# Optimization experiments

Hardware: AMD Instinct MI355X
Metric: run time of the kernel (lower is better)

## Reference

```python
import jax, jax.numpy as jnp
import numpy as np

N_NODES, NUM_FEAT, EMB, HID, N_CLASSES, N_EDGES = 800, 111, 32, 200, 15, 8000
ALPHA = 0.5   # DirGNNConv default mixing
EPS = 1e-5    # LayerNorm eps


def _pade_coeffs(deg=5):
    # [5/5] Pade approximant of sqrt(1 - x) (as in FastDifferentiableMatSqrt)
    K = 2 * deg + 1
    b = np.zeros(K); b[0] = 1.0
    for k in range(1, K):
        b[k] = b[k - 1] * (0.5 - (k - 1)) / k
    c = b * ((-1.0) ** np.arange(K))  # Taylor coeffs of sqrt(1-x)
    A = np.empty((deg, deg))
    for i in range(deg):
        for j in range(1, deg + 1):
            A[i, j - 1] = c[deg + 1 + i - j]
    q = np.concatenate([[1.0], np.linalg.solve(A, -c[deg + 1:])])
    p = np.array([sum(q[j] * c[k - j] for j in range(min(k, deg) + 1)) for k in range(deg + 1)])
    return p.astype(np.float32), q.astype(np.float32)

PADE_P, PADE_Q = _pade_coeffs()


def _mpa_impl(A):
    # matrix square root via Pade approximant (MPA forward)
    normA = jnp.sqrt(jnp.sum(A * A))
    I = jnp.eye(A.shape[0], dtype=A.dtype)
    p_app = I - A / normA
    p_hat = p_app
    p_sqrt = PADE_P[0] * I
    q_sqrt = PADE_Q[0] * I
    for i in range(5):
        p_sqrt = p_sqrt + PADE_P[i + 1] * p_hat
        q_sqrt = q_sqrt + PADE_Q[i + 1] * p_hat
        p_hat = p_hat @ p_app
    return jnp.linalg.solve(q_sqrt, p_sqrt) * jnp.sqrt(normA)


@jax.custom_vjp
def mpa_lya(A):
    return _mpa_impl(A)


def _mpa_fwd(A):
    S = _mpa_impl(A)
    return S, (S, jnp.sqrt(jnp.sum(A * A)))


def _mpa_bwd(res, g):
    # iterative Lyapunov solver backward (8 coupled Newton-Schulz iterations)
    S, normA = res
    I = jnp.eye(S.shape[0], dtype=S.dtype)
    b = S / jnp.sqrt(normA)
    c = g / jnp.sqrt(normA)
    for _ in range(8):
        b2 = b @ b
        c = 0.5 * (c @ (3.0 * I - b2) - b2 @ c + b @ (c @ b))
        b = 0.5 * (b @ (3.0 * I - b2))
    return (0.5 * c,)

mpa_lya.defvjp(_mpa_fwd, _mpa_bwd)


def gcn_sparse(m, ei, n):
    # GCNConv(normalize=False): out[dst] = sum_{(src,dst) in E} (x @ W)[src]
    return jax.ops.segment_sum(m[ei[0]], ei[1], num_segments=n)


def hetero_layer_sparse(h, eis, W, b):
    # W: [3(in,out,root), 4 edge types, Fin, Fout]; HeteroConv aggr='sum'
    n = h.shape[0]
    out = jnp.zeros((n, W.shape[-1]), h.dtype)
    for e, ei in enumerate(eis):
        x_in = gcn_sparse(h @ W[0, e], ei, n) + b[0, e]
        x_out = gcn_sparse(h @ W[1, e], ei[::-1], n) + b[1, e]  # flipped edges
        out = out + ALPHA * x_out + (1.0 - ALPHA) * x_in + h @ W[2, e] + b[2, e]
    return out


def hetero_layer_dense(h, masks, W, b):
    # masks: [4, N, N] binary adjacency (src, dst); dense equivalent of scatter
    out = jnp.zeros((h.shape[0], W.shape[-1]), h.dtype)
    for e in range(masks.shape[0]):
        x_in = masks[e].T @ (h @ W[0, e]) + b[0, e]
        x_out = masks[e] @ (h @ W[1, e]) + b[1, e]
        out = out + ALPHA * x_out + (1.0 - ALPHA) * x_in + h @ W[2, e] + b[2, e]
    return out


def graph_layernorm(h, wb):
    # PyG LayerNorm mode='graph', single graph: normalize over all nodes+feats
    mu = jnp.mean(h)
    var = jnp.mean((h - mu) ** 2)
    return (h - mu) / jnp.sqrt(var + EPS) * wb[0] + wb[1]


def hetero_gnn(h, layer_fn, graph, W1, b1, W2, b2, ln):
    h = graph_layernorm(layer_fn(h, graph, W1, b1), ln[0])
    return graph_layernorm(layer_fn(h, graph, W2, b2), ln[1])


def pairwise_S(z, lin_W, lin_b, iu, ju):
    n = z.shape[0]
    M = (z[iu] - z[ju]) ** 2                        # [N(N+1)/2, HID]
    mg = jax.nn.sigmoid(M @ lin_W + lin_b)[:, 0]    # upper-tri entries, row-major
    tri = jnp.zeros((n, n), z.dtype).at[iu, ju].set(mg)
    return mpa_lya(tri)


def model_forward(x_note, embed_W, embed_b, g1_l1_W, g1_l1_b, g1_l2_W, g1_l2_b, g1_ln,
                  g2_l1_W, g2_l1_b, g2_l2_W, g2_l2_b, g2_ln, lin_W, lin_b, clf_W, clf_b,
                  eis, batch):
    n = x_note.shape[0]
    iu, ju = np.triu_indices(n)
    h = x_note @ embed_W + embed_b                   # [N, 32]
    z0 = hetero_gnn(h, hetero_layer_sparse, eis, g1_l1_W, g1_l1_b, g1_l2_W, g1_l2_b, g1_ln)
    S1 = pairwise_S(z0, lin_W, lin_b, iu, ju)
    A0 = jnp.stack([jnp.zeros((n, n), h.dtype).at[ei[0], ei[1]].set(1.0) for ei in eis])
    h = S1 @ h
    # adj_to_coord(nonzero) only keeps the binary pattern of S1 @ A @ S1
    mask1 = jnp.stack([((S1 @ A0[e]) @ S1 != 0).astype(h.dtype) for e in range(4)])
    z1 = hetero_gnn(h, hetero_layer_dense, mask1, g2_l1_W, g2_l1_b, g2_l2_W, g2_l2_b, g2_ln)
    S2 = pairwise_S(z1, lin_W, lin_b, iu, ju)
    h = S2 @ h
    mask2 = jnp.stack([((S2 @ mask1[e]) @ S2 != 0).astype(h.dtype) for e in range(4)])
    z2 = hetero_gnn(h, hetero_layer_dense, mask2, g2_l1_W, g2_l1_b, g2_l2_W, g2_l2_b, g2_ln)
    counts = jax.ops.segment_sum(jnp.ones((n,), z2.dtype), batch, num_segments=1)
    x2 = jax.ops.segment_sum(z2, batch, num_segments=1) / counts[:, None]  # global_mean_pool
    logits = x2 @ clf_W + clf_b
    return x2, jax.nn.log_softmax(logits, axis=-1), S1, S2


def setup_inputs() -> dict:
    key = jax.random.key(0)
    ks = jax.random.split(key, 14)
    N, F, E, H, NC, NE = N_NODES, NUM_FEAT, EMB, HID, N_CLASSES, N_EDGES
    def w(k, shape, fan_in):
        return (jax.random.normal(k, shape, jnp.float32) / np.sqrt(fan_in)).astype(jnp.float32)
    ln = jnp.broadcast_to(jnp.stack([jnp.ones(H, jnp.float32), jnp.zeros(H, jnp.float32)]), (2, 2, H)) + 0.0
    return dict(
        x_note=jax.random.normal(ks[0], (N, F), jnp.float32),
        embed_W=w(ks[1], (F, E), F), embed_b=jnp.zeros((E,), jnp.float32),
        g1_l1_W=w(ks[2], (3, 4, E, H), E), g1_l1_b=jnp.zeros((3, 4, H), jnp.float32),
        g1_l2_W=w(ks[3], (3, 4, H, H), H), g1_l2_b=jnp.zeros((3, 4, H), jnp.float32),
        g1_ln=ln,
        g2_l1_W=w(ks[4], (3, 4, E, H), E), g2_l1_b=jnp.zeros((3, 4, H), jnp.float32),
        g2_l2_W=w(ks[5], (3, 4, H, H), H), g2_l2_b=jnp.zeros((3, 4, H), jnp.float32),
        g2_ln=ln,
        lin_W=w(ks[6], (H, 1), H), lin_b=jnp.zeros((1,), jnp.float32),
        clf_W=w(ks[7], (H, NC), H), clf_b=jnp.zeros((NC,), jnp.float32),
        ei_forward=jax.random.randint(ks[8], (2, NE), 0, N, jnp.int32),
        ei_onset=jax.random.randint(ks[9], (2, NE), 0, N, jnp.int32),
        ei_sustain=jax.random.randint(ks[10], (2, NE), 0, N, jnp.int32),
        ei_rest=jax.random.randint(ks[11], (2, NE), 0, N, jnp.int32),
        batch=jnp.zeros((N,), jnp.int32),
    )


def reference(x_note, embed_W, embed_b, g1_l1_W, g1_l1_b, g1_l2_W, g1_l2_b, g1_ln,
              g2_l1_W, g2_l1_b, g2_l2_W, g2_l2_b, g2_ln, lin_W, lin_b, clf_W, clf_b,
              ei_forward, ei_onset, ei_sustain, ei_rest, batch):
    eis = (ei_forward, ei_onset, ei_sustain, ei_rest)
    return model_forward(x_note, embed_W, embed_b, g1_l1_W, g1_l1_b, g1_l2_W, g1_l2_b, g1_ln,
                         g2_l1_W, g2_l1_b, g2_l2_W, g2_l2_b, g2_ln, lin_W, lin_b, clf_W, clf_b,
                         eis, batch)
```

## Files before the change

kernel.cpp:

```cpp
#include <hip/hip_runtime.h>
#include <hip/hip_bf16.h>
#include <math.h>
#include <stdio.h>

static constexpr int   kN  = 800;
static constexpr int   kF  = 111;
static constexpr int   kE  = 32;
static constexpr int   kH  = 200;
static constexpr int   kNC = 15;
static constexpr int   kNE = 8000;
static constexpr long  kNN = (long)kN*kN;
static constexpr long  kNH = (long)kN*kH;
static constexpr float kAl  = 0.5f;
static constexpr float kEps = 1e-5f;
static constexpr int   kGB  = (int)((kNH+255)/256);
static constexpr int   kDB  = 50;

typedef unsigned short u16;
typedef __attribute__((ext_vector_type(8))) short short8;
typedef __attribute__((ext_vector_type(4))) float f32x4;

__device__ __forceinline__ u16 f2bf(float v){
  __hip_bfloat16 b = __float2bfloat16(v);
  return *reinterpret_cast<u16*>(&b);
}
__device__ __forceinline__ float bf2f(u16 h){
  unsigned int u = ((unsigned int)h) << 16;
  float f; __builtin_memcpy(&f, &u, 4);
  return f;
}

enum { EPI_NONE=0, EPI_BIAS=1, EPI_SCALE=4, EPI_ACC=6 };

template<bool TRANSA, bool TRIUA, bool TRIUB, int EPI>
__global__ __launch_bounds__(256)
void gemm_kernel(const float* __restrict__ A, int lda,
                 const float* __restrict__ B, int ldb,
                 float* __restrict__ C, int ldc,
                 int M, int Ncl, int K,
                 long sA, long sB, long sC, float scale,
                 const float* __restrict__ bias, int kstep,
                 const double* __restrict__ scalp)
{
  constexpr int TM=64, TN=64, TK=16;
  A += (long)blockIdx.z * sA;
  B += (long)blockIdx.z * sB;
  C += (long)blockIdx.z * sC;
  __shared__ float As[TK][TM+4];
  __shared__ float Bs[TK][TN+4];
  const int tid = threadIdx.x;
  const int tn4 = (tid & 15)*4, tm4 = (tid >> 4)*4;
  const int m0 = blockIdx.x * TM, n0 = blockIdx.y * TN;
  float acc[4][4] = {};
  const int kbase = kstep ? (int)blockIdx.z * kstep : 0;
  int k0 = TRIUA ? max(m0 - kbase, 0) : 0;
  int kEnd = TRIUB ? min(K, n0 + TN - kbase) : K;
  const bool skip = (k0 >= kEnd);
  if (skip && EPI == EPI_ACC) return;
  if (!skip) {
    float ar[4], br[4];
    auto loadT = [&](int kk0, float* arr, float* brr){
      #pragma unroll
      for (int u=0; u<4; ++u){
        int idx = tid + 256*u;
        float av;
        if (!TRANSA) {
          int m = idx >> 4, ka = idx & 15;
          int gm = m0+m, gk = kk0+ka;
          av = (gm < M && gk < K) ? A[(long)gm*lda + gk] : 0.f;
        } else {
          int ka = idx >> 6, m = idx & 63;
          int gm = m0+m, gk = kk0+ka;
          av = (gm < M && gk < K) ? A[(long)gk*lda + gm] : 0.f;
        }
        int kb = idx >> 6, nb = idx & 63;
        int gk = kk0+kb, gn = n0+nb;
        arr[u] = av;
        brr[u] = (gk < K && gn < Ncl) ? B[(long)gk*ldb + gn] : 0.f;
      }
    };
    auto storeT = [&](const float* arr, const float* brr){
      #pragma unroll
      for (int u=0; u<4; ++u){
        int idx = tid + 256*u;
        if (!TRANSA){ int m = idx>>4, ka = idx&15; As[ka][m] = arr[u]; }
        else        { int ka = idx>>6, m = idx&63; As[ka][m] = arr[u]; }
        int kb = idx>>6, nb = idx&63;
        Bs[kb][nb] = brr[u];
      }
    };
    loadT(k0, ar, br);
    for (;;){
      __syncthreads();
      storeT(ar, br);
      __syncthreads();
      int kn = k0 + TK;
      bool more = kn < kEnd;
      if (more) loadT(kn, ar, br);
      #pragma unroll
      for (int kk=0; kk<TK; ++kk) {
        float a[4], b[4];
        #pragma unroll
        for (int u=0;u<4;++u){ a[u]=As[kk][tm4+u]; b[u]=Bs[kk][tn4+u]; }
        #pragma unroll
        for (int i=0;i<4;++i)
          #pragma unroll
          for (int j=0;j<4;++j)
            acc[i][j] = fmaf(a[i], b[j], acc[i][j]);
      }
      if (!more) break;
      k0 = kn;
    }
  }
  float sc = scale;
  if (EPI == EPI_ACC && scalp) sc *= (float)sqrt(sqrt(scalp[0]));
  #pragma unroll
  for (int i=0;i<4;++i) {
    int gm = m0 + tm4 + i;
    if (gm >= M) continue;
    #pragma unroll
    for (int j=0;j<4;++j) {
      int gn = n0 + tn4 + j;
      if (gn >= Ncl) continue;
      float v = acc[i][j];
      long off = (long)gm*ldc + gn;
      if (EPI == EPI_BIAS)       C[off] = v + bias[gn];
      else if (EPI == EPI_SCALE) C[off] = scale*v;
      else if (EPI == EPI_ACC)   unsafeAtomicAdd(&C[off], sc*v);
      else                       C[off] = v;
    }
  }
}

template<bool TRANSA, bool TRIUA, bool TRIUB, int EPI>
static inline void launch_gemm(hipStream_t st,
                               const float* A, int lda, const float* B, int ldb,
                               float* C, int ldc, int M, int Ncl, int K, int batch,
                               long sA, long sB, long sC, float scale,
                               const float* bias = nullptr, int kstep = 0,
                               const double* scalp = nullptr)
{
  dim3 grid((M+63)/64, (Ncl+63)/64, batch);
  gemm_kernel<TRANSA,TRIUA,TRIUB,EPI><<<grid, 256, 0, st>>>(
      A,lda,B,ldb,C,ldc,M,Ncl,K,sA,sB,sC,scale,bias,kstep,scalp);
}

__global__ __launch_bounds__(256)
void bgemm2_kernel(const u16* __restrict__ Ah, const u16* __restrict__ Al,
                   const u16* __restrict__ Bh, const u16* __restrict__ Bl,
                   float* __restrict__ C, float* __restrict__ C2,
                   u16* __restrict__ Oh, u16* __restrict__ Ol,
                   float p0, float p1)
{
  constexpr int TM=64, TN=64, BK=32;
  __shared__ u16 Ash[TM][40], Asl[TM][40], Bsh[TN][40], Bsl[TN][40];
  const int tid = threadIdx.x;
  const int m0 = blockIdx.x*TM, n0 = blockIdx.y*TN;
  const int w = tid>>6, lane = tid&63;
  const int wm = (w&1)*32, wn = (w>>1)*32;
  const int quad = lane>>4, lm = lane&15;
  f32x4 acc00={}, acc01={}, acc10={}, acc11={};
  const bool skip = (m0 > n0 + TN - 1);
  int k0 = m0;
  const int kEnd = min(kN, n0+TN);
  const int ar = tid>>2, ac = (tid&3)*8;
  if (!skip){
    uint4 avh, avl, bvh, bvl;
    auto loadT = [&](int kk0){
      avh = {0,0,0,0}; avl = {0,0,0,0}; bvh = {0,0,0,0}; bvl = {0,0,0,0};
      int gk = kk0 + ac;
      if (m0+ar < kN && gk < kN){
        avh = *(const uint4*)(Ah + (long)(m0+ar)*kN + gk);
        avl = *(const uint4*)(Al + (long)(m0+ar)*kN + gk);
      }
      if (n0+ar < kN && gk < kN){
        bvh = *(const uint4*)(Bh + (long)(n0+ar)*kN + gk);
        bvl = *(const uint4*)(Bl + (long)(n0+ar)*kN + gk);
      }
    };
    loadT(k0);
    for (;;){
      __syncthreads();
      *(uint4*)&Ash[ar][ac] = avh; *(uint4*)&Asl[ar][ac] = avl;
      *(uint4*)&Bsh[ar][ac] = bvh; *(uint4*)&Bsl[ar][ac] = bvl;
      __syncthreads();
      int kn = k0 + BK;
      bool more = kn < kEnd;
      if (more) loadT(kn);
      short8 a0h = *(const short8*)&Ash[wm+lm][quad*8];
      short8 a1h = *(const short8*)&Ash[wm+16+lm][quad*8];
      short8 a0l = *(const short8*)&Asl[wm+lm][quad*8];
      short8 a1l = *(const short8*)&Asl[wm+16+lm][quad*8];
      short8 b0h = *(const short8*)&Bsh[wn+lm][quad*8];
      short8 b1h = *(const short8*)&Bsh[wn+16+lm][quad*8];
      short8 b0l = *(const short8*)&Bsl[wn+lm][quad*8];
      short8 b1l = *(const short8*)&Bsl[wn+16+lm][quad*8];
      acc00 = __builtin_amdgcn_mfma_f32_16x16x32_bf16(a0h,b0h,acc00,0,0,0);
      acc00 = __builtin_amdgcn_mfma_f32_16x16x32_bf16(a0h,b0l,acc00,0,0,0);
      acc00 = __builtin_amdgcn_mfma_f32_16x16x32_bf16(a0l,b0h,acc00,0,0,0);
      acc01 = __builtin_amdgcn_mfma_f32_16x16x32_bf16(a0h,b1h,acc01,0,0,0);
      acc01 = __builtin_amdgcn_mfma_f32_16x16x32_bf16(a0h,b1l,acc01,0,0,0);
      acc01 = __builtin_amdgcn_mfma_f32_16x16x32_bf16(a0l,b1h,acc01,0,0,0);
      acc10 = __builtin_amdgcn_mfma_f32_16x16x32_bf16(a1h,b0h,acc10,0,0,0);
      acc10 = __builtin_amdgcn_mfma_f32_16x16x32_bf16(a1h,b0l,acc10,0,0,0);
      acc10 = __builtin_amdgcn_mfma_f32_16x16x32_bf16(a1l,b0h,acc10,0,0,0);
      acc11 = __builtin_amdgcn_mfma_f32_16x16x32_bf16(a1h,b1h,acc11,0,0,0);
      acc11 = __builtin_amdgcn_mfma_f32_16x16x32_bf16(a1h,b1l,acc11,0,0,0);
      acc11 = __builtin_amdgcn_mfma_f32_16x16x32_bf16(a1l,b1h,acc11,0,0,0);
      if (!more) break;
      k0 = kn;
    }
  }
  f32x4 accs[2][2] = {{acc00, acc01},{acc10, acc11}};
  #pragma unroll
  for (int ti=0; ti<2; ++ti){
    #pragma unroll
    for (int tj=0; tj<2; ++tj){
      #pragma unroll
      for (int r=0; r<4; ++r){
        int gm = m0 + wm + ti*16 + quad*4 + r;
        int gn = n0 + wn + tj*16 + lm;
        if (gm >= kN || gn >= kN) continue;
        float v = accs[ti][tj][r];
        long off = (long)gm*kN + gn;
        C[off]  += p0*v;
        C2[off] += p1*v;
        u16 h = f2bf(v);
        Oh[off] = h;
        Ol[off] = f2bf(v - bf2f(h));
      }
    }
  }
}

__global__ __launch_bounds__(256)
void pade_both_kernel(const float* __restrict__ tri, const double* __restrict__ frob2,
                      u16* __restrict__ ph, u16* __restrict__ pl,
                      u16* __restrict__ th, u16* __restrict__ tl,
                      float* __restrict__ psq, float* __restrict__ qsq,
                      float P0, float P1, float Q0, float Q1)
{
  __shared__ float t[32][33];
  const float rn = (float)(1.0 / sqrt(frob2[0]));
  int r0 = blockIdx.y*32, c0 = blockIdx.x*32;
  int tr = threadIdx.x>>5, tc = threadIdx.x&31;
  for (int i=tr; i<32; i+=8){
    int r = r0+i, c = c0+tc;
    float eye = (r==c) ? 1.f : 0.f;
    float pa = eye - tri[(long)r*kN + c]*rn;
    t[i][tc] = pa;
    long off = (long)r*kN + c;
    psq[off] = P0*eye + P1*pa;
    qsq[off] = Q0*eye + Q1*pa;
    u16 h = f2bf(pa);
    ph[off] = h;
    pl[off] = f2bf(pa - bf2f(h));
  }
  __syncthreads();
  for (int i=tr; i<32; i+=8){
    int c = c0+i, r = r0+tc;
    float v = t[tc][i];
    u16 h = f2bf(v);
    th[(long)c*kN + r] = h;
    tl[(long)c*kN + r] = f2bf(v - bf2f(h));
  }
}

__global__ __launch_bounds__(256)
void copy_scale_kernel(const float* __restrict__ src, const double* __restrict__ frob2,
                       float* __restrict__ dst)
{
  const float fac = (float)sqrt(sqrt(frob2[0]));
  long i = (long)blockIdx.x*256 + threadIdx.x;
  if (i < kNN) __builtin_nontemporal_store(src[i]*fac, &dst[i]);
}

__global__ void edge_count_kernel(const int* __restrict__ e0, const int* __restrict__ e1,
                                  const int* __restrict__ e2, const int* __restrict__ e3,
                                  int* __restrict__ cnt){
  const int* eis[4] = {e0,e1,e2,e3};
  const int e = blockIdx.y;
  const int* ei = eis[e];
  int j = blockIdx.x*256 + threadIdx.x;
  if (j >= kNE) return;
  int s = ei[j], d = ei[kNE + j];
  atomicAdd(&cnt[e*kN + d], 1);
  atomicAdd(&cnt[(4+e)*kN + s], 1);
}

__global__ void csr_scan_kernel(const int* __restrict__ cnt, int* __restrict__ offs,
                                int* __restrict__ cur){
  const int l = blockIdx.x;
  if (threadIdx.x != 0) return;
  int acc = 0;
  for (int i = 0; i < kN; ++i){
    offs[l*(kN+1) + i] = acc;
    cur[l*kN + i] = acc;
    acc += cnt[l*kN + i];
  }
  offs[l*(kN+1) + kN] = acc;
}

__global__ void edge_fill_kernel(const int* __restrict__ e0, const int* __restrict__ e1,
                                 const int* __restrict__ e2, const int* __restrict__ e3,
                                 int* __restrict__ cur, int* __restrict__ adj){
  const int* eis[4] = {e0,e1,e2,e3};
  const int e = blockIdx.y;
  const int* ei = eis[e];
  int j = blockIdx.x*256 + threadIdx.x;
  if (j >= kNE) return;
  int s = ei[j], d = ei[kNE + j];
  int p = atomicAdd(&cur[e*kN + d], 1);
  adj[(long)e*kNE + p] = s;
  int q = atomicAdd(&cur[(4+e)*kN + s], 1);
  adj[(long)(4+e)*kNE + q] = d;
}

__global__ __launch_bounds__(256)
// ... 54 lines not shown
  for (int i = threadIdx.x; i < kN; i += 256) g[e*kN + i] = gs[i];
  for (int d = threadIdx.x; d < kN; d += 256){
    int lo = 0, hi = kN;
    while (lo < hi){ int mid = (lo+hi)>>1; if (gs[mid] >= d) hi = mid; else lo = mid+1; }
    h[e*kN + d] = lo;
  }
}

__global__ __launch_bounds__(256)
void scan_msg_kernel(float* __restrict__ Y){
  const int plane = blockIdx.x;
  const int f = threadIdx.x;
  if (f >= kH) return;
  float* P = Y + (long)plane*kNH + f;
  float acc = 0.f;
  if (plane < 4){
    for (int n = 0; n < kN; n += 4){
      float v0 = P[(long)(n+0)*kH], v1 = P[(long)(n+1)*kH];
      float v2 = P[(long)(n+2)*kH], v3 = P[(long)(n+3)*kH];
      acc += v0; P[(long)(n+0)*kH] = acc;
      acc += v1; P[(long)(n+1)*kH] = acc;
      acc += v2; P[(long)(n+2)*kH] = acc;
      acc += v3; P[(long)(n+3)*kH] = acc;
    }
  } else {
    for (int n = kN-1; n >= 0; n -= 4){
      float v0 = P[(long)(n-0)*kH], v1 = P[(long)(n-1)*kH];
      float v2 = P[(long)(n-2)*kH], v3 = P[(long)(n-3)*kH];
      acc += v0; P[(long)(n-0)*kH] = acc;
      acc += v1; P[(long)(n-1)*kH] = acc;
      acc += v2; P[(long)(n-2)*kH] = acc;
      acc += v3; P[(long)(n-3)*kH] = acc;
    }
  }
}

__global__ __launch_bounds__(256)
void gather_dense_kernel(const float* __restrict__ Y, const int* __restrict__ g,
                         const int* __restrict__ h, const float* __restrict__ bsum,
                         float* __restrict__ tnh, double* __restrict__ part){
  __shared__ double ss[256], qq[256];
  long idx = (long)blockIdx.x*256 + threadIdx.x;
  double s = 0.0, q = 0.0;
  if (idx < kNH){
    int n = (int)(idx / kH), f = (int)(idx % kH);
    float v = 0.f;
    #pragma unroll
    for (int e = 0; e < 4; ++e){
      int gi = g[e*kN + n];
      if (gi >= 0) v += Y[(long)e*kNH + (long)gi*kH + f];
      int hi = h[e*kN + n];
      if (hi < kN) v += Y[(long)(4+e)*kNH + (long)hi*kH + f];
    }
    float t = Y[(long)8*kNH + idx] + bsum[f] + 0.5f*v;
    tnh[idx] = t;
    s = t; q = (double)t*t;
  }
  ss[threadIdx.x]=s; qq[threadIdx.x]=q;
  __syncthreads();
  for (int hh=128; hh>0; hh>>=1){
    if ((int)threadIdx.x < hh){ ss[threadIdx.x]+=ss[threadIdx.x+hh]; qq[threadIdx.x]+=qq[threadIdx.x+hh]; }
    __syncthreads();
  }
  if (threadIdx.x==0){ part[2*blockIdx.x]=ss[0]; part[2*blockIdx.x+1]=qq[0]; }
}

__global__ void sum_root_kernel(const float* __restrict__ W, const float* __restrict__ b,
                                int K, float* __restrict__ Wr, float* __restrict__ bsum){
  int idx = blockIdx.x*256 + threadIdx.x;
  int tot = K*kH;
  if (idx < tot){
    float v = 0.f;
    #pragma unroll
    for (int e=0;e<4;++e) v += W[(long)(8+e)*tot + idx];
    Wr[idx] = v;
  }
  if (idx < kH){
    float v = 0.f;
    #pragma unroll
    for (int e=0;e<4;++e)
      v += (1.f-kAl)*b[(0*4+e)*kH + idx] + kAl*b[(1*4+e)*kH + idx] + b[(2*4+e)*kH + idx];
    bsum[idx] = v;
  }
}

__global__ __launch_bounds__(256)
void apply_ln_kernel(const float* __restrict__ x, float* __restrict__ y,
                     const float* __restrict__ ln, const double* __restrict__ part, int nb){
  __shared__ double ss[256], qq[256];
  int t = threadIdx.x;
  double s=0.0, q=0.0;
  for (int i=t; i<nb; i+=256){ s += part[2*i]; q += part[2*i+1]; }
  ss[t]=s; qq[t]=q;
  __syncthreads();
  for (int h=128; h>0; h>>=1){
    if (t < h){ ss[t]+=ss[t+h]; qq[t]+=qq[t+h]; }
    __syncthreads();
  }
  long idx = (long)blockIdx.x*256 + t;
  if (idx >= kNH) return;
  double mu  = ss[0] / (double)kNH;
  double var = qq[0] / (double)kNH - mu*mu;
  float rs = rsqrtf((float)var + kEps);
  int f = (int)(idx % kH);
  y[idx] = (x[idx] - (float)mu) * rs * ln[f] + ln[kH + f];
}

__global__ __launch_bounds__(256)
void pair_kernel(const float* __restrict__ zraw, const double* __restrict__ part, int nb,
                 const float* __restrict__ ln,
                 const float* __restrict__ linW, const float* __restrict__ linb,
                 float* __restrict__ tri, double* __restrict__ frob2){
  __shared__ float zi[16][201], zj[16][201], w[208], lw[208], lb[208];
  __shared__ float red[256];
  __shared__ double sred[256], qred[256];
  const int i0 = blockIdx.y*16, j0 = blockIdx.x*16;
  const int tid = threadIdx.x;
  const int ti = tid >> 4, tj = tid & 15;
  const int i = i0+ti, j = j0+tj;
  if (i0 > j0 + 15) { tri[(long)i*kN + j] = 0.f; return; }
  double s=0.0, q=0.0;
  for (int ii=tid; ii<nb; ii+=256){ s += part[2*ii]; q += part[2*ii+1]; }
  sred[tid]=s; qred[tid]=q;
  __syncthreads();
  for (int hh=128; hh>0; hh>>=1){
    if (tid < hh){ sred[tid]+=sred[tid+hh]; qred[tid]+=qred[tid+hh]; }
    __syncthreads();
  }
  const float mu = (float)(sred[0] / (double)kNH);
  const float rs = rsqrtf((float)(qred[0]/(double)kNH - (sred[0]/(double)kNH)*(sred[0]/(double)kNH)) + kEps);
  if (tid < kH){ w[tid] = linW[tid]; lw[tid] = ln[tid]; lb[tid] = ln[kH + tid]; }
  __syncthreads();
  for (int idx = tid; idx < 16*kH; idx += 256){
    int r = idx / kH, c = idx % kH;
    float sc = rs*lw[c], of = lb[c];
    zi[r][c] = (zraw[(long)(i0+r)*kH + c] - mu)*sc + of;
    zj[r][c] = (zraw[(long)(j0+r)*kH + c] - mu)*sc + of;
  }
  __syncthreads();
  float g = 0.f;
  if (i <= j){
    float sacc = linb[0];
    #pragma unroll 4
    for (int k=0;k<kH;++k){ float d = zi[ti][k]-zj[tj][k]; sacc = fmaf(d*d, w[k], sacc); }
    g = 1.f/(1.f + expf(-sacc));
  }
  tri[(long)i*kN + j] = g;
  red[tid] = g*g;
  __syncthreads();
  for (int hh=128; hh>0; hh>>=1){
    if (tid < hh) red[tid] += red[tid+hh];
    __syncthreads();
  }
  if (tid == 0) unsafeAtomicAdd(frob2, (double)red[0]);
}

__global__ __launch_bounds__(64)
void invdiag_kernel(const float* __restrict__ U, float* __restrict__ W){
  __shared__ float Us[kDB][kDB+1];
  __shared__ float Xs[kDB][kDB+1];
  const int base = blockIdx.x * kDB;
  const int tid = threadIdx.x;
  for (int idx = tid; idx < kDB*kDB; idx += 64){
    int r = idx / kDB, c = idx % kDB;
    Us[r][c] = U[(long)(base+r)*kN + base + c];
  }
  __syncthreads();
  const int c = tid;
  for (int i = kDB-1; i >= 0; --i){
    if (c < kDB){
      float x;
      if (c < i) x = 0.f;
      else {
        float s = 0.f;
        for (int k = i+1; k < kDB; ++k) s = fmaf(Us[i][k], Xs[k][c], s);
        x = (((c==i)?1.f:0.f) - s) / Us[i][i];
      }
      Xs[i][c] = x;
    }
    __syncthreads();
  }
  for (int idx = tid; idx < kDB*kDB; idx += 64){
    int r = idx / kDB, cc = idx % kDB;
    W[(long)(base+r)*kN + base + cc] = Xs[r][cc];
  }
}

template<int S>
__global__ __launch_bounds__(256)
void merge_fused_kernel(const float* __restrict__ U, float* __restrict__ W){
  __shared__ float Us[S][S+1];
  __shared__ float Wb[S][S+1];
  __shared__ float T[S][S+1];
  const long base = (long)blockIdx.x * (2*S) * (kN+1);
  const int tid = threadIdx.x;
  for (int idx = tid; idx < S*S; idx += 256){
    int r = idx / S, c = idx % S;
    Us[r][c] = U[base + (long)r*kN + S + c];
    Wb[r][c] = W[base + (long)(S+r)*kN + S + c];
  }
  __syncthreads();
  for (int idx = tid; idx < S*S; idx += 256){
    int r = idx / S, c = idx % S;
    float s = 0.f;
    for (int k = 0; k <= c; ++k) s = fmaf(Us[r][k], Wb[k][c], s);
    T[r][c] = s;
  }
  __syncthreads();
  for (int idx = tid; idx < S*S; idx += 256){
    int r = idx / S, c = idx % S;
    Us[r][c] = W[base + (long)r*kN + c];
  }
  __syncthreads();
  for (int idx = tid; idx < S*S; idx += 256){
    int r = idx / S, c = idx % S;
    float s = 0.f;
    for (int k = r; k < S; ++k) s = fmaf(Us[r][k], T[k][c], s);
    W[base + (long)r*kN + S + c] = -s;
  }
}

__global__ __launch_bounds__(256)
void pool_head_kernel(const float* __restrict__ z2raw, const double* __restrict__ part, int nb,
                      const float* __restrict__ ln,
                      const float* __restrict__ W, const float* __restrict__ b,
                      float* __restrict__ out){
  __shared__ double sred[256], qred[256];
  __shared__ float x2[kH];
  __shared__ float lg[kNC];
  int t = threadIdx.x;
  double s=0.0, q=0.0;
  for (int i=t; i<nb; i+=256){ s += part[2*i]; q += part[2*i+1]; }
  sred[t]=s; qred[t]=q;
  __syncthreads();
  for (int hh=128; hh>0; hh>>=1){
    if (t < hh){ sred[t]+=sred[t+hh]; qred[t]+=qred[t+hh]; }
    __syncthreads();
// ... 11 lines not shown
  __syncthreads();
  if (t < kNC){
    float sv = b[t];
    for (int f = 0; f < kH; ++f) sv = fmaf(x2[f], W[f*kNC + t], sv);
    lg[t] = sv;
  }
  __syncthreads();
  if (t == 0){
    float m = -1e30f;
    for (int c=0;c<kNC;++c) m = fmaxf(m, lg[c]);
    float se = 0.f;
    for (int c=0;c<kNC;++c) se += expf(lg[c]-m);
    float lse = m + logf(se);
    for (int c=0;c<kNC;++c) out[kH + c] = lg[c]-lse;
  }
}

static void pade_coeffs(float* P, float* Q){
  double b[11]; b[0] = 1.0;
  for (int k=1;k<11;++k) b[k] = b[k-1]*(0.5-(k-1))/k;
  double c[11];
  for (int k=0;k<11;++k) c[k] = b[k]*((k&1)?-1.0:1.0);
  double A[5][5], rhs[5];
  for (int i=0;i<5;++i){ for (int j=0;j<5;++j) A[i][j] = c[5+i-j]; rhs[i] = -c[6+i]; }
  for (int col=0; col<5; ++col){
    int p = col;
    for (int r=col+1;r<5;++r) if (fabs(A[r][col]) > fabs(A[p][col])) p = r;
    if (p != col){
      for (int j=0;j<5;++j){ double t=A[col][j]; A[col][j]=A[p][j]; A[p][j]=t; }
      double t=rhs[col]; rhs[col]=rhs[p]; rhs[p]=t;
    }
    for (int r=col+1;r<5;++r){
      double f = A[r][col]/A[col][col];
      for (int j=col;j<5;++j) A[r][j] -= f*A[col][j];
      rhs[r] -= f*rhs[col];
    }
  }
  double q[6]; q[0] = 1.0;
  for (int r=4;r>=0;--r){
    double s = rhs[r];
    for (int j=r+1;j<5;++j) s -= A[r][j]*q[1+j];
    q[1+r] = s/A[r][r];
  }
  double p[6];
  for (int k=0;k<6;++k){
    double s = 0.0; int jm = k<5?k:5;
    for (int j=0;j<=jm;++j) s += q[j]*c[k-j];
    p[k] = s;
  }
  for (int k=0;k<6;++k){ P[k]=(float)p[k]; Q[k]=(float)q[k]; }
}

extern "C" void kernel_launch(void* const* d_in, const int* in_sizes, int n_in,
                              void* d_out, int out_size, void* d_ws, size_t ws_size,
                              hipStream_t stream)
{
  const float* x_note = (const float*)d_in[0];
  const float* embW   = (const float*)d_in[1];
  const float* embB   = (const float*)d_in[2];
  const float* g1w1   = (const float*)d_in[3];
  const float* g1b1   = (const float*)d_in[4];
  const float* g1w2   = (const float*)d_in[5];
  const float* g1b2   = (const float*)d_in[6];
  const float* g1ln   = (const float*)d_in[7];
  const float* g2w1   = (const float*)d_in[8];
  const float* g2b1   = (const float*)d_in[9];
  const float* g2w2   = (const float*)d_in[10];
  const float* g2b2   = (const float*)d_in[11];
  const float* g2ln   = (const float*)d_in[12];
  const float* linW   = (const float*)d_in[13];
  const float* linb   = (const float*)d_in[14];
  const float* clfW   = (const float*)d_in[15];
  const float* clfb   = (const float*)d_in[16];
  const int*  e0     = (const int*)d_in[17];
  const int*  e1     = (const int*)d_in[18];
  const int*  e2     = (const int*)d_in[19];
  const int*  e3     = (const int*)d_in[20];
  float* out = (float*)d_out;

  constexpr long o_h0   = 4096;
  constexpr long o_h1   = o_h0   + (long)kN*kE;
  constexpr long o_h2   = o_h1   + (long)kN*kE;
  constexpr long o_tnh  = o_h2   + (long)kN*kE;
  constexpr long o_zmid = o_tnh  + kNH;
  constexpr long o_big  = o_zmid + kNH;
  constexpr long o_tri  = o_big  + 4*kNN;
  constexpr long o_sacc = o_tri  + kNN;
  constexpr long o_winv = o_sacc + kNN;
  constexpr long o_psq  = o_winv + kNN;
  constexpr long o_qsq  = o_psq  + kNN;
  constexpr long o_g    = o_qsq  + kNN;
  constexpr long o_hh   = o_g    + 4*kN;
  constexpr long o_wc1  = o_hh   + 4*kN;
  constexpr long o_wc2  = o_wc1  + 9L*kE*kH;
  constexpr long o_wc3  = o_wc2  + 9L*kH*kH;
  constexpr long o_wc4  = o_wc3  + 9L*kE*kH;
  constexpr long o_bs   = o_wc4  + 9L*kH*kH;
  constexpr long o_cnt  = o_bs   + 4*kH;
  constexpr long o_offs = o_cnt  + 8*kN;
  constexpr long o_cur  = o_offs + 8*(kN+1);
  constexpr long o_adj  = o_cur  + 8*kN;
  constexpr long o_end  = o_adj  + 8*(long)kNE;

  if (ws_size < (size_t)o_end*sizeof(float) || out_size < 215 + 2*(int)kNN || n_in < 21){
    fprintf(stderr, "kernel_launch guard: ws=%zu need=%zu out=%d need=%d n_in=%d\n",
            ws_size, (size_t)o_end*sizeof(float), out_size, (int)(215+2*kNN), n_in);
    hipMemsetAsync(d_out, 0, (size_t)out_size*sizeof(float), stream);
    return;
  }

  float* ws = (float*)d_ws;
  double* scald = (double*)d_ws;
  double* partd = (double*)((char*)d_ws + 512);
  float *h0=ws+o_h0, *h1=ws+o_h1, *h2=ws+o_h2, *tnh=ws+o_tnh, *zmid=ws+o_zmid,
        *big=ws+o_big, *tri=ws+o_tri, *Sacc=ws+o_sacc, *winv=ws+o_winv,
        *psq=ws+o_psq, *qsq=ws+o_qsq;
  int* gArr = (int*)(ws + o_g);
  int* hArr = (int*)(ws + o_hh);
  float *wc1=ws+o_wc1, *wc2=ws+o_wc2, *wc3=ws+o_wc3, *wc4=ws+o_wc4, *bs=ws+o_bs;
  int* cntA = (int*)(ws + o_cnt);
  int* offsA= (int*)(ws + o_offs);
  int* curA = (int*)(ws + o_cur);
  int* adjA = (int*)(ws + o_adj);
  u16* papp_h = (u16*)big;
  u16* papp_l = papp_h + kNN;
  u16* pT_h   = papp_l + kNN;
  u16* pT_l   = pT_h + kNN;
  u16* pwA_h  = pT_l + kNN;
  u16* pwA_l  = pwA_h + kNN;
  u16* pwB_h  = pwA_l + kNN;
  u16* pwB_l  = pwB_h + kNN;

  float P[6], Q[6];
  pade_coeffs(P, Q);

  auto eg = [](long n){ return dim3((unsigned)((n+255)/256)); };

  auto layer_gemm = [&](const float* hin, int K, const float* wcat){
    launch_gemm<false,false,false,EPI_NONE>(stream, hin, K, wcat, kH, big, kH, kN, kH, K, 9,
                                            0, (long)K*kH, kNH, 0.f);
  };
  auto sparse_layer = [&](const float* hin, int K, const float* wcat, const float* bsum){
    layer_gemm(hin, K, wcat);
    gather_sparse_kernel<<<dim3(kN),256,0,stream>>>(big, offsA, adjA, bsum, tnh, partd);
  };
  auto dense_layer = [&](const float* hin, int K, const float* wcat, const float* bsum){
    layer_gemm(hin, K, wcat);
    scan_msg_kernel<<<8,256,0,stream>>>(big);
    gather_dense_kernel<<<kGB,256,0,stream>>>(big, gArr, hArr, bsum, tnh, partd);
  };
  auto blocked_trsm = [&](){
    hipMemsetAsync(winv, 0, (size_t)kNN*sizeof(float), stream);
    invdiag_kernel<<<dim3(kN/kDB),64,0,stream>>>(qsq, winv);
    merge_fused_kernel<50><<<dim3(kN/100),256,0,stream>>>(qsq, winv);
    {
      int s = 100, npairs = 4;
      long step = (long)2*s*kN + 2*s;
      launch_gemm<false,false,true,EPI_NONE>(stream,
          qsq + s, kN, winv + (long)s*kN + s, kN, tri, s,
          s, s, s, npairs, step, step, (long)s*s, 0.f);
      launch_gemm<false,true,false,EPI_SCALE>(stream,
          winv, kN, tri, s, winv + s, kN,
          s, s, s, npairs, step, (long)s*s, step, -1.f);
    }
    {
      int s = 200, npairs = 2;
      long step = (long)2*s*kN + 2*s;
      launch_gemm<false,false,true,EPI_NONE>(stream,
          qsq + s, kN, winv + (long)s*kN + s, kN, tri, s,
          s, s, s, npairs, step, step, (long)s*s, 0.f);
      launch_gemm<false,true,false,EPI_SCALE>(stream,
          winv, kN, tri, s, winv + s, kN,
          s, s, s, npairs, step, (long)s*s, step, -1.f);
    }
    {
      hipMemsetAsync(tri, 0, (size_t)400*400*sizeof(float), stream);
      launch_gemm<false,false,true,EPI_ACC>(stream,
          qsq + 400, kN, winv + (long)400*kN + 400, kN, tri, 400,
          400, 400, 100, 4, 100, (long)100*kN, 0, 1.f, nullptr, 100);
      launch_gemm<false,true,false,EPI_ACC>(stream,
          winv, kN, tri, 400, winv + 400, kN,
          400, 400, 100, 4, 100, (long)100*400, 0, -1.f, nullptr, 100);
    }
    hipMemsetAsync(Sacc, 0, (size_t)kNN*sizeof(float), stream);
    launch_gemm<false,true,true,EPI_ACC>(stream,
        winv, kN, psq, kN, Sacc, kN, kN, kN, 100, 8,
        100, (long)100*kN, 0, 1.f, nullptr, 100);
  };
  auto run_pair_mpa = [&](int nb, const float* lnp, float* SoutDst){
    hipMemsetAsync((char*)d_ws + 24, 0, 8, stream);
    pair_kernel<<<dim3(50,50),256,0,stream>>>(tnh, partd, nb, lnp, linW, linb, tri, scald+3);
    pade_both_kernel<<<dim3(25,25),256,0,stream>>>(tri, scald+3, papp_h, papp_l, pT_h, pT_l,
                                                   psq, qsq, P[0],P[1],Q[0],Q[1]);
    dim3 g13(13,13,1);
    bgemm2_kernel<<<g13,256,0,stream>>>(papp_h,papp_l, pT_h,pT_l, psq,qsq, pwA_h,pwA_l, P[2],Q[2]);
    bgemm2_kernel<<<g13,256,0,stream>>>(pwA_h,pwA_l,  pT_h,pT_l, psq,qsq, pwB_h,pwB_l, P[3],Q[3]);
    bgemm2_kernel<<<g13,256,0,stream>>>(pwB_h,pwB_l,  pT_h,pT_l, psq,qsq, pwA_h,pwA_l, P[4],Q[4]);
    bgemm2_kernel<<<g13,256,0,stream>>>(pwA_h,pwA_l,  pT_h,pT_l, psq,qsq, pwB_h,pwB_l, P[5],Q[5]);
    blocked_trsm();
    copy_scale_kernel<<<eg(kNN),256,0,stream>>>(Sacc, scald+3, SoutDst);
  };
  auto s_times_h = [&](const float* hin, float* hout){
    hipMemsetAsync(hout, 0, (size_t)kN*kE*sizeof(float), stream);
    launch_gemm<false,true,false,EPI_ACC>(stream,
        Sacc, kN, hin, kE, hout, kE, kN, kE, 100, 8,
        100, (long)100*kE, 0, 1.f, nullptr, 100, scald+3);
  };

  float* S1f = out + 215;
  float* S2f = out + 215 + kNN;

  hipMemsetAsync(gArr, 0xFF, (size_t)(4*kN)*sizeof(int), stream);
  edge_gmax_kernel<<<dim3((kNE+255)/256,4),256,0,stream>>>(e0,e1,e2,e3, gArr);
  scan_gh_kernel<<<4,256,0,stream>>>(gArr, hArr);
  hipMemsetAsync(cntA, 0, (size_t)(8*kN)*sizeof(int), stream);
  edge_count_kernel<<<dim3((kNE+255)/256,4),256,0,stream>>>(e0,e1,e2,e3, cntA);
  csr_scan_kernel<<<8,64,0,stream>>>(cntA, offsA, curA);
  edge_fill_kernel<<<dim3((kNE+255)/256,4),256,0,stream>>>(e0,e1,e2,e3, curA, adjA);
  hipMemcpyAsync(wc1, g1w1, 8L*kE*kH*sizeof(float), hipMemcpyDeviceToDevice, stream);
  hipMemcpyAsync(wc2, g1w2, 8L*kH*kH*sizeof(float), hipMemcpyDeviceToDevice, stream);
  hipMemcpyAsync(wc3, g2w1, 8L*kE*kH*sizeof(float), hipMemcpyDeviceToDevice, stream);
  hipMemcpyAsync(wc4, g2w2, 8L*kH*kH*sizeof(float), hipMemcpyDeviceToDevice, stream);
  sum_root_kernel<<<eg((long)kE*kH),256,0,stream>>>(g1w1, g1b1, kE, wc1 + 8L*kE*kH, bs);
  sum_root_kernel<<<eg((long)kH*kH),256,0,stream>>>(g1w2, g1b2, kH, wc2 + 8L*kH*kH, bs+kH);
  sum_root_kernel<<<eg((long)kE*kH),256,0,stream>>>(g2w1, g2b1, kE, wc3 + 8L*kE*kH, bs+2*kH);
  sum_root_kernel<<<eg((long)kH*kH),256,0,stream>>>(g2w2, g2b2, kH, wc4 + 8L*kH*kH, bs+3*kH);

  launch_gemm<false,false,false,EPI_BIAS>(stream, x_note, kF, embW, kE, h0, kE, kN, kE, kF, 1,
                                          0,0,0, 0.f, embB);

  sparse_layer(h0, kE, wc1, bs);
  apply_ln_kernel<<<eg(kNH),256,0,stream>>>(tnh, zmid, g1ln, partd, kN);
  sparse_layer(zmid, kH, wc2, bs+kH);

  run_pair_mpa(kN, g1ln + 2*kH, S1f);

  s_times_h(h0, h1);

  dense_layer(h1, kE, wc3, bs+2*kH);
  apply_ln_kernel<<<eg(kNH),256,0,stream>>>(tnh, zmid, g2ln, partd, kGB);
  dense_layer(zmid, kH, wc4, bs+3*kH);

  run_pair_mpa(kGB, g2ln + 2*kH, S2f);

  s_times_h(h1, h2);

  dense_layer(h2, kE, wc3, bs+2*kH);
  apply_ln_kernel<<<eg(kNH),256,0,stream>>>(tnh, zmid, g2ln, partd, kGB);
  dense_layer(zmid, kH, wc4, bs+3*kH);

  pool_head_kernel<<<dim3(1),256,0,stream>>>(tnh, partd, kGB, g2ln + 2*kH, clfW, clfb, out);
}
```

Measured before the change: 1.136 ms.

## Fuse LayerNorm into GEMM A-loads and compute pair kernel via bf16 MFMA GEMM

Removes the standalone apply_ln_kernel by applying the LayerNorm on the fly inside the layer GEMM's A-tile loads; each block recomputes the global mean and variance from the partial sums. It also replaces the scalar pairwise-distance kernel with an algebraic expansion, sum w(zi-zj)^2 = a_i + a_j - 2*(w*zi)·zj. The cross term runs as a split-bf16 (hi/lo) MFMA GEMM, fed by a per-row prep kernel that normalizes and splits the features. The cost is a redundant stats reduction in every GEMM block and some cancellation error from the expanded-square form.

```diff
diff --git a/kernel.cpp b/kernel.cpp
--- a/kernel.cpp
+++ b/kernel.cpp
@@ -32,7 +32,7 @@
 
 enum { EPI_NONE=0, EPI_BIAS=1, EPI_SCALE=4, EPI_ACC=6 };
 
-template<bool TRANSA, bool TRIUA, bool TRIUB, int EPI>
+template<bool TRANSA, bool TRIUA, bool TRIUB, int EPI, bool LNA>
 __global__ __launch_bounds__(256)
 void gemm_kernel(const float* __restrict__ A, int lda,
                  const float* __restrict__ B, int ldb,
@@ -40,7 +40,9 @@
                  int M, int Ncl, int K,
                  long sA, long sB, long sC, float scale,
                  const float* __restrict__ bias, int kstep,
-                 const double* __restrict__ scalp)
+                 const double* __restrict__ scalp,
+                 const float* __restrict__ lnw,
+                 const double* __restrict__ lnpart, int lnnb)
 {
   constexpr int TM=64, TN=64, TK=16;
   A += (long)blockIdx.z * sA;
@@ -52,6 +54,23 @@
   const int tn4 = (tid & 15)*4, tm4 = (tid >> 4)*4;
   const int m0 = blockIdx.x * TM, n0 = blockIdx.y * TN;
   float acc[4][4] = {};
+  float mu = 0.f, rsf = 1.f;
+  if (LNA){
+    __shared__ double lnS[256], lnQ[256];
+    double s=0.0, q=0.0;
+    for (int i=tid; i<lnnb; i+=256){ s += lnpart[2*i]; q += lnpart[2*i+1]; }
+    lnS[tid]=s; lnQ[tid]=q;
+    __syncthreads();
+    for (int h=128; h>0; h>>=1){
+      if (tid < h){ lnS[tid]+=lnS[tid+h]; lnQ[tid]+=lnQ[tid+h]; }
+      __syncthreads();
+    }
+    double m = lnS[0]/(double)kNH;
+    double var = lnQ[0]/(double)kNH - m*m;
+    mu = (float)m;
+    rsf = rsqrtf((float)var + kEps);
+    __syncthreads();
+  }
   const int kbase = kstep ? (int)blockIdx.z * kstep : 0;
   int k0 = TRIUA ? max(m0 - kbase, 0) : 0;
   int kEnd = TRIUB ? min(K, n0 + TN - kbase) : K;
@@ -63,15 +82,21 @@
       #pragma unroll
       for (int u=0; u<4; ++u){
         int idx = tid + 256*u;
-        float av;
+        float av = 0.f;
         if (!TRANSA) {
           int m = idx >> 4, ka = idx & 15;
           int gm = m0+m, gk = kk0+ka;
-          av = (gm < M && gk < K) ? A[(long)gm*lda + gk] : 0.f;
+          if (gm < M && gk < K){
+            av = A[(long)gm*lda + gk];
+            if (LNA) av = (av - mu)*(rsf*lnw[gk]) + lnw[kH + gk];
+          }
         } else {
           int ka = idx >> 6, m = idx & 63;
           int gm = m0+m, gk = kk0+ka;
-          av = (gm < M && gk < K) ? A[(long)gk*lda + gm] : 0.f;
+          if (gm < M && gk < K){
+            av = A[(long)gk*lda + gm];
+            if (LNA) av = (av - mu)*(rsf*lnw[gk]) + lnw[kH + gk];
+          }
         }
         int kb = idx >> 6, nb = idx & 63;
         int gk = kk0+kb, gn = n0+nb;
@@ -132,17 +157,19 @@
   }
 }
 
-template<bool TRANSA, bool TRIUA, bool TRIUB, int EPI>
+template<bool TRANSA, bool TRIUA, bool TRIUB, int EPI, bool LNA = false>
 static inline void launch_gemm(hipStream_t st,
                                const float* A, int lda, const float* B, int ldb,
                                float* C, int ldc, int M, int Ncl, int K, int batch,
                                long sA, long sB, long sC, float scale,
                                const float* bias = nullptr, int kstep = 0,
-                               const double* scalp = nullptr)
+                               const double* scalp = nullptr,
+                               const float* lnw = nullptr,
+                               const double* lnpart = nullptr, int lnnb = 0)
 {
   dim3 grid((M+63)/64, (Ncl+63)/64, batch);
-  gemm_kernel<TRANSA,TRIUA,TRIUB,EPI><<<grid, 256, 0, st>>>(
-      A,lda,B,ldb,C,ldc,M,Ncl,K,sA,sB,sC,scale,bias,kstep,scalp);
+  gemm_kernel<TRANSA,TRIUA,TRIUB,EPI,LNA><<<grid, 256, 0, st>>>(
+      A,lda,B,ldb,C,ldc,M,Ncl,K,sA,sB,sC,scale,bias,kstep,scalp,lnw,lnpart,lnnb);
 }
 
 __global__ __launch_bounds__(256)
@@ -234,6 +261,139 @@
 }
 
 __global__ __launch_bounds__(256)
+void ln_pair_prep_kernel(const float* __restrict__ tnh, const double* __restrict__ part,
+                         int nb, const float* __restrict__ ln, const float* __restrict__ linW,
+                         u16* __restrict__ zwh, u16* __restrict__ zwl,
+                         u16* __restrict__ zzh, u16* __restrict__ zzl,
+                         float* __restrict__ avec)
+{
+  __shared__ double ss[256], qq[256];
+  __shared__ float ared[256];
+  const int n = blockIdx.x, t = threadIdx.x;
+  double s=0.0, q=0.0;
+  for (int i=t; i<nb; i+=256){ s += part[2*i]; q += part[2*i+1]; }
+  ss[t]=s; qq[t]=q;
+  __syncthreads();
+  for (int h=128; h>0; h>>=1){
+    if (t < h){ ss[t]+=ss[t+h]; qq[t]+=qq[t+h]; }
+    __syncthreads();
+  }
+  double m = ss[0]/(double)kNH;
+  const float mu = (float)m;
+  const float rs = rsqrtf((float)(qq[0]/(double)kNH - m*m) + kEps);
+  float acc = 0.f;
+  if (t < kH){
+    float z = (tnh[(long)n*kH + t] - mu)*(rs*ln[t]) + ln[kH + t];
+    float wv = linW[t];
+    float zw = wv*z;
+    long off = (long)n*kH + t;
+    u16 h1 = f2bf(zw);
+    zwh[off] = h1; zwl[off] = f2bf(zw - bf2f(h1));
+    u16 h2 = f2bf(z);
+    zzh[off] = h2; zzl[off] = f2bf(z - bf2f(h2));
+    acc = zw*z;
+  }
+  ared[t] = acc;
+  __syncthreads();
+  for (int h=128; h>0; h>>=1){
+    if (t < h) ared[t] += ared[t+h];
+    __syncthreads();
+  }
+  if (t == 0) avec[n] = ared[0];
+}
+
+__global__ __launch_bounds__(256)
+void bgemm_pair_kernel(const u16* __restrict__ Ah, const u16* __restrict__ Al,
+                       const u16* __restrict__ Bh, const u16* __restrict__ Bl,
+                       const float* __restrict__ avec, const float* __restrict__ linb,
+                       float* __restrict__ tri, double* __restrict__ frob2)
+{
+  constexpr int TM=64, TN=64, BK=32, KK=kH;
+  __shared__ u16 Ash[TM][40], Asl[TM][40], Bsh[TN][40], Bsl[TN][40];
+  __shared__ float red[256];
+  const int tid = threadIdx.x;
+  const int m0 = blockIdx.x*TM, n0 = blockIdx.y*TN;
+  if (m0 > n0 + TN - 1){
+    for (int idx = tid; idx < TM*TN; idx += 256){
+      int r = idx >> 6, c = idx & 63;
+      int gm = m0 + r, gn = n0 + c;
+      if (gm < kN && gn < kN) tri[(long)gm*kN + gn] = 0.f;
+    }
+    return;
+  }
+  const int w = tid>>6, lane = tid&63;
+  const int wm = (w&1)*32, wn = (w>>1)*32;
+  const int quad = lane>>4, lm = lane&15;
+  f32x4 acc00={}, acc01={}, acc10={}, acc11={};
+  const int ar = tid>>2, ac = (tid&3)*8;
+  for (int k0 = 0; k0 < KK; k0 += BK){
+    uint4 avh={0,0,0,0}, avl={0,0,0,0}, bvh={0,0,0,0}, bvl={0,0,0,0};
+    int gk = k0 + ac;
+    if (m0+ar < kN && gk < KK){
+      avh = *(const uint4*)(Ah + (long)(m0+ar)*KK + gk);
+      avl = *(const uint4*)(Al + (long)(m0+ar)*KK + gk);
+    }
+    if (n0+ar < kN && gk < KK){
+      bvh = *(const uint4*)(Bh + (long)(n0+ar)*KK + gk);
+      bvl = *(const uint4*)(Bl + (long)(n0+ar)*KK + gk);
+    }
+    __syncthreads();
+    *(uint4*)&Ash[ar][ac] = avh; *(uint4*)&Asl[ar][ac] = avl;
+    *(uint4*)&Bsh[ar][ac] = bvh; *(uint4*)&Bsl[ar][ac] = bvl;
+    __syncthreads();
+    short8 a0h = *(const short8*)&Ash[wm+lm][quad*8];
+    short8 a1h = *(const short8*)&Ash[wm+16+lm][quad*8];
+    short8 a0l = *(const short8*)&Asl[wm+lm][quad*8];
+    short8 a1l = *(const short8*)&Asl[wm+16+lm][quad*8];
+    short8 b0h = *(const short8*)&Bsh[wn+lm][quad*8];
+    short8 b1h = *(const short8*)&Bsh[wn+16+lm][quad*8];
+    short8 b0l = *(const short8*)&Bsl[wn+lm][quad*8];
+    short8 b1l = *(const short8*)&Bsl[wn+16+lm][quad*8];
+    acc00 = __builtin_amdgcn_mfma_f32_16x16x32_bf16(a0h,b0h,acc00,0,0,0);
+    acc00 = __builtin_amdgcn_mfma_f32_16x16x32_bf16(a0h,b0l,acc00,0,0,0);
+    acc00 = __builtin_amdgcn_mfma_f32_16x16x32_bf16(a0l,b0h,acc00,0,0,0);
+    acc01 = __builtin_amdgcn_mfma_f32_16x16x32_bf16(a0h,b1h,acc01,0,0,0);
+    acc01 = __builtin_amdgcn_mfma_f32_16x16x32_bf16(a0h,b1l,acc01,0,0,0);
+    acc01 = __builtin_amdgcn_mfma_f32_16x16x32_bf16(a0l,b1h,acc01,0,0,0);
+    acc10 = __builtin_amdgcn_mfma_f32_16x16x32_bf16(a1h,b0h,acc10,0,0,0);
+    acc10 = __builtin_amdgcn_mfma_f32_16x16x32_bf16(a1h,b0l,acc10,0,0,0);
+    acc10 = __builtin_amdgcn_mfma_f32_16x16x32_bf16(a1l,b0h,acc10,0,0,0);
+    acc11 = __builtin_amdgcn_mfma_f32_16x16x32_bf16(a1h,b1h,acc11,0,0,0);
+    acc11 = __builtin_amdgcn_mfma_f32_16x16x32_bf16(a1h,b1l,acc11,0,0,0);
+    acc11 = __builtin_amdgcn_mfma_f32_16x16x32_bf16(a1l,b1h,acc11,0,0,0);
+  }
+  const float lb = linb[0];
+  float r2 = 0.f;
+  f32x4 accs[2][2] = {{acc00, acc01},{acc10, acc11}};
+  #pragma unroll
+  for (int ti=0; ti<2; ++ti){
+    #pragma unroll
+    for (int tj=0; tj<2; ++tj){
+      #pragma unroll
+      for (int r=0; r<4; ++r){
+        int gm = m0 + wm + ti*16 + quad*4 + r;
+        int gn = n0 + wn + tj*16 + lm;
+        if (gm >= kN || gn >= kN) continue;
+        float t = 0.f;
+        if (gm <= gn){
+          float marg = avec[gm] + avec[gn] - 2.f*accs[ti][tj][r] + lb;
+          t = 1.f/(1.f + expf(-marg));
+        }
+        tri[(long)gm*kN + gn] = t;
+        r2 += t*t;
+      }
+    }
+  }
+  red[tid] = r2;
+  __syncthreads();
+  for (int h=128; h>0; h>>=1){
+    if (tid < h) red[tid] += red[tid+h];
+    __syncthreads();
+  }
+  if (tid == 0) unsafeAtomicAdd(frob2, (double)red[0]);
+}
+
+__global__ __launch_bounds__(256)
 void pade_both_kernel(const float* __restrict__ tri, const double* __restrict__ frob2,
                       u16* __restrict__ ph, u16* __restrict__ pl,
                       u16* __restrict__ th, u16* __restrict__ tl,
@@ -454,77 +614,6 @@
       v += (1.f-kAl)*b[(0*4+e)*kH + idx] + kAl*b[(1*4+e)*kH + idx] + b[(2*4+e)*kH + idx];
     bsum[idx] = v;
   }
-}
-
-__global__ __launch_bounds__(256)
-void apply_ln_kernel(const float* __restrict__ x, float* __restrict__ y,
-                     const float* __restrict__ ln, const double* __restrict__ part, int nb){
-  __shared__ double ss[256], qq[256];
-  int t = threadIdx.x;
-  double s=0.0, q=0.0;
-  for (int i=t; i<nb; i+=256){ s += part[2*i]; q += part[2*i+1]; }
-  ss[t]=s; qq[t]=q;
-  __syncthreads();
-  for (int h=128; h>0; h>>=1){
-    if (t < h){ ss[t]+=ss[t+h]; qq[t]+=qq[t+h]; }
-    __syncthreads();
-  }
-  long idx = (long)blockIdx.x*256 + t;
-  if (idx >= kNH) return;
-  double mu  = ss[0] / (double)kNH;
-  double var = qq[0] / (double)kNH - mu*mu;
-  float rs = rsqrtf((float)var + kEps);
-  int f = (int)(idx % kH);
-  y[idx] = (x[idx] - (float)mu) * rs * ln[f] + ln[kH + f];
-}
-
-__global__ __launch_bounds__(256)
-void pair_kernel(const float* __restrict__ zraw, const double* __restrict__ part, int nb,
-                 const float* __restrict__ ln,
-                 const float* __restrict__ linW, const float* __restrict__ linb,
-                 float* __restrict__ tri, double* __restrict__ frob2){
-  __shared__ float zi[16][201], zj[16][201], w[208], lw[208], lb[208];
-  __shared__ float red[256];
-  __shared__ double sred[256], qred[256];
-  const int i0 = blockIdx.y*16, j0 = blockIdx.x*16;
-  const int tid = threadIdx.x;
-  const int ti = tid >> 4, tj = tid & 15;
-  const int i = i0+ti, j = j0+tj;
-  if (i0 > j0 + 15) { tri[(long)i*kN + j] = 0.f; return; }
-  double s=0.0, q=0.0;
-  for (int ii=tid; ii<nb; ii+=256){ s += part[2*ii]; q += part[2*ii+1]; }
-  sred[tid]=s; qred[tid]=q;
-  __syncthreads();
-  for (int hh=128; hh>0; hh>>=1){
-    if (tid < hh){ sred[tid]+=sred[tid+hh]; qred[tid]+=qred[tid+hh]; }
-    __syncthreads();
-  }
-  const float mu = (float)(sred[0] / (double)kNH);
-  const float rs = rsqrtf((float)(qred[0]/(double)kNH - (sred[0]/(double)kNH)*(sred[0]/(double)kNH)) + kEps);
-  if (tid < kH){ w[tid] = linW[tid]; lw[tid] = ln[tid]; lb[tid] = ln[kH + tid]; }
-  __syncthreads();
-  for (int idx = tid; idx < 16*kH; idx += 256){
-    int r = idx / kH, c = idx % kH;
-    float sc = rs*lw[c], of = lb[c];
-    zi[r][c] = (zraw[(long)(i0+r)*kH + c] - mu)*sc + of;
-    zj[r][c] = (zraw[(long)(j0+r)*kH + c] - mu)*sc + of;
-  }
-  __syncthreads();
-  float g = 0.f;
-  if (i <= j){
-    float sacc = linb[0];
-    #pragma unroll 4
-    for (int k=0;k<kH;++k){ float d = zi[ti][k]-zj[tj][k]; sacc = fmaf(d*d, w[k], sacc); }
-    g = 1.f/(1.f + expf(-sacc));
-  }
-  tri[(long)i*kN + j] = g;
-  red[tid] = g*g;
-  __syncthreads();
-  for (int hh=128; hh>0; hh>>=1){
-    if (tid < hh) red[tid] += red[tid+hh];
-    __syncthreads();
-  }
-  if (tid == 0) unsafeAtomicAdd(frob2, (double)red[0]);
 }
 
 __global__ __launch_bounds__(64)
@@ -702,8 +791,9 @@
   constexpr long o_h1   = o_h0   + (long)kN*kE;
   constexpr long o_h2   = o_h1   + (long)kN*kE;
   constexpr long o_tnh  = o_h2   + (long)kN*kE;
-  constexpr long o_zmid = o_tnh  + kNH;
-  constexpr long o_big  = o_zmid + kNH;
+  constexpr long o_pp   = o_tnh  + kNH;
+  constexpr long o_av   = o_pp   + 2*kNH;
+  constexpr long o_big  = o_av   + kN;
   constexpr long o_tri  = o_big  + 4*kNN;
   constexpr long o_sacc = o_tri  + kNN;
   constexpr long o_winv = o_sacc + kNN;
@@ -732,9 +822,14 @@
   float* ws = (float*)d_ws;
   double* scald = (double*)d_ws;
   double* partd = (double*)((char*)d_ws + 512);
-  float *h0=ws+o_h0, *h1=ws+o_h1, *h2=ws+o_h2, *tnh=ws+o_tnh, *zmid=ws+o_zmid,
+  float *h0=ws+o_h0, *h1=ws+o_h1, *h2=ws+o_h2, *tnh=ws+o_tnh,
         *big=ws+o_big, *tri=ws+o_tri, *Sacc=ws+o_sacc, *winv=ws+o_winv,
         *psq=ws+o_psq, *qsq=ws+o_qsq;
+  u16* zwh = (u16*)(ws + o_pp);
+  u16* zwl = zwh + kNH;
+  u16* zzh = zwl + kNH;
+  u16* zzl = zzh + kNH;
+  float* avec = ws + o_av;
   int* gArr = (int*)(ws + o_g);
   int* hArr = (int*)(ws + o_hh);
   float *wc1=ws+o_wc1, *wc2=ws+o_wc2, *wc3=ws+o_wc3, *wc4=ws+o_wc4, *bs=ws+o_bs;
@@ -756,16 +851,23 @@
 
   auto eg = [](long n){ return dim3((unsigned)((n+255)/256)); };
 
-  auto layer_gemm = [&](const float* hin, int K, const float* wcat){
-    launch_gemm<false,false,false,EPI_NONE>(stream, hin, K, wcat, kH, big, kH, kN, kH, K, 9,
-                                            0, (long)K*kH, kNH, 0.f);
+  auto layer_gemm = [&](const float* hin, int K, const float* wcat,
+                        const float* lnp, int nb){
+    if (lnp)
+      launch_gemm<false,false,false,EPI_NONE,true>(stream, hin, K, wcat, kH, big, kH,
+          kN, kH, K, 9, 0, (long)K*kH, kNH, 0.f, nullptr, 0, nullptr, lnp, partd, nb);
+    else
+      launch_gemm<false,false,false,EPI_NONE>(stream, hin, K, wcat, kH, big, kH,
+          kN, kH, K, 9, 0, (long)K*kH, kNH, 0.f);
   };
-  auto sparse_layer = [&](const float* hin, int K, const float* wcat, const float* bsum){
-    layer_gemm(hin, K, wcat);
+  auto sparse_layer = [&](const float* hin, int K, const float* wcat, const float* bsum,
+                          const float* lnp, int nb){
+    layer_gemm(hin, K, wcat, lnp, nb);
     gather_sparse_kernel<<<dim3(kN),256,0,stream>>>(big, offsA, adjA, bsum, tnh, partd);
   };
-  auto dense_layer = [&](const float* hin, int K, const float* wcat, const float* bsum){
-    layer_gemm(hin, K, wcat);
+  auto dense_layer = [&](const float* hin, int K, const float* wcat, const float* bsum,
+                         const float* lnp, int nb){
+    layer_gemm(hin, K, wcat, lnp, nb);
     scan_msg_kernel<<<8,256,0,stream>>>(big);
     gather_dense_kernel<<<kGB,256,0,stream>>>(big, gArr, hArr, bsum, tnh, partd);
   };
@@ -809,7 +911,10 @@
   };
   auto run_pair_mpa = [&](int nb, const float* lnp, float* SoutDst){
     hipMemsetAsync((char*)d_ws + 24, 0, 8, stream);
-    pair_kernel<<<dim3(50,50),256,0,stream>>>(tnh, partd, nb, lnp, linW, linb, tri, scald+3);
+    ln_pair_prep_kernel<<<dim3(kN),256,0,stream>>>(tnh, partd, nb, lnp, linW,
+                                                   zwh, zwl, zzh, zzl, avec);
+    bgemm_pair_kernel<<<dim3(13,13),256,0,stream>>>(zwh, zwl, zzh, zzl, avec, linb,
+                                                    tri, scald+3);
     pade_both_kernel<<<dim3(25,25),256,0,stream>>>(tri, scald+3, papp_h, papp_l, pT_h, pT_l,
                                                    psq, qsq, P[0],P[1],Q[0],Q[1]);
     dim3 g13(13,13,1);
@@ -849,25 +954,22 @@
   launch_gemm<false,false,false,EPI_BIAS>(stream, x_note, kF, embW, kE, h0, kE, kN, kE, kF, 1,
                                           0,0,0, 0.f, embB);
 
-  sparse_layer(h0, kE, wc1, bs);
-  apply_ln_kernel<<<eg(kNH),256,0,stream>>>(tnh, zmid, g1ln, partd, kN);
-  sparse_layer(zmid, kH, wc2, bs+kH);
+  sparse_layer(h0,  kE, wc1, bs,      nullptr, 0);
+  sparse_layer(tnh, kH, wc2, bs+kH,   g1ln, kN);
 
   run_pair_mpa(kN, g1ln + 2*kH, S1f);
 
   s_times_h(h0, h1);
 
-  dense_layer(h1, kE, wc3, bs+2*kH);
-  apply_ln_kernel<<<eg(kNH),256,0,stream>>>(tnh, zmid, g2ln, partd, kGB);
-  dense_layer(zmid, kH, wc4, bs+3*kH);
+  dense_layer(h1,  kE, wc3, bs+2*kH, nullptr, 0);
+  dense_layer(tnh, kH, wc4, bs+3*kH, g2ln, kGB);
 
   run_pair_mpa(kGB, g2ln + 2*kH, S2f);
 
   s_times_h(h1, h2);
 
-  dense_layer(h2, kE, wc3, bs+2*kH);
-  apply_ln_kernel<<<eg(kNH),256,0,stream>>>(tnh, zmid, g2ln, partd, kGB);
-  dense_layer(zmid, kH, wc4, bs+3*kH);
+  dense_layer(h2,  kE, wc3, bs+2*kH, nullptr, 0);
+  dense_layer(tnh, kH, wc4, bs+3*kH, g2ln, kGB);
 
   pool_head_kernel<<<dim3(1),256,0,stream>>>(tnh, partd, kGB, g2ln + 2*kH, clfW, clfb, out);
 }
```

Result: no change. 1.122 ms (-1.3%).
